# Optimization experiments

Hardware: AMD Instinct MI355X
Metric: run time of the kernel (lower is better)

## Reference

```python
import jax, jax.numpy as jnp
import numpy as np

B, DIM, HEADS, H, W = 4, 64, 8, 512, 512


def _conv(x, w, groups=1):
    # NCHW x, OIHW w, stride 1, SAME padding (padding=k//2 in torch)
    return jax.lax.conv_general_dilated(
        x, w, (1, 1), 'SAME', feature_group_count=groups,
        dimension_numbers=('NCHW', 'OIHW', 'NCHW'))


def _dwt_haar(x):
    # single-level orthonormal haar on even-sized NCHW input
    a = x[..., 0::2, 0::2]; b = x[..., 0::2, 1::2]
    c = x[..., 1::2, 0::2]; d = x[..., 1::2, 1::2]
    LL = (a + b + c + d) * 0.5
    LH = (-a - b + c + d) * 0.5
    HL = (-a + b - c + d) * 0.5
    HH = (a - b - c + d) * 0.5
    return LL, LH, HL, HH


def _idwt_haar(LL, LH, HL, HH):
    a = (LL - LH - HL + HH) * 0.5
    b = (LL - LH + HL - HH) * 0.5
    c = (LL + LH - HL - HH) * 0.5
    d = (LL + LH + HL + HH) * 0.5
    Bn, C, h, w = LL.shape
    even = jnp.stack([a, b], -1).reshape(Bn, C, h, 2 * w)  # rows 0::2
    odd = jnp.stack([c, d], -1).reshape(Bn, C, h, 2 * w)   # rows 1::2
    return jnp.stack([even, odd], -2).reshape(Bn, C, 2 * h, 2 * w)


def _l2norm(x, eps=1e-12):
    n = jnp.sqrt(jnp.sum(x * x, axis=-1, keepdims=True))
    return x / jnp.maximum(n, eps)


def setup_inputs() -> dict:
    key = jax.random.key(0)
    ks = jax.random.split(key, 8)
    def w(k, shape):
        fan_in = shape[1] * shape[2] * shape[3]
        return jax.random.normal(k, shape, jnp.float32) * (1.0 / np.sqrt(fan_in))
    return {
        'x': jax.random.normal(ks[0], (B, DIM, H, W), jnp.float32),
        'w_hc1': w(ks[1], (2 * DIM, DIM, 3, 3)),        # groups=2 over 2*dim channels
        'w_hc2': w(ks[2], (DIM, 2 * DIM, 1, 1)),
        'w_ho': w(ks[3], (3 * DIM, DIM, 3, 3)),          # groups=3 over 3*dim channels
        'w_qkv': w(ks[4], (3 * DIM, DIM, 1, 1)),
        'w_dw': w(ks[5], (3 * DIM, 1, 3, 3)),            # depthwise, groups=3*dim
        'w_proj': w(ks[6], (DIM, DIM, 1, 1)),
        'temperature': jnp.ones((HEADS, 1, 1), jnp.float32),
    }


def reference(x, w_hc1, w_hc2, w_ho, w_qkv, w_dw, w_proj, temperature):
    LL, LH, HL, HH = _dwt_haar(x)

    # high-frequency (LH,HL) filter branch
    hv = jnp.concatenate([LH, HL], axis=1)
    filter_hv = jax.nn.relu(_conv(jax.nn.relu(_conv(hv, w_hc1, groups=2)), w_hc2))

    # qkv from LL: 1x1 conv then depthwise 3x3
    qkv = _conv(_conv(LL, w_qkv), w_dw, groups=3 * DIM)
    q, k, v = jnp.split(qkv, 3, axis=1)
    b, c, h, w = q.shape
    v = v * filter_hv + v

    ch = c // HEADS
    q = q.reshape(b, HEADS, ch, h * w)
    k = k.reshape(b, HEADS, ch, h * w)
    v = v.reshape(b, HEADS, ch, h * w)
    q = _l2norm(q)
    k = _l2norm(k)

    attn = jnp.einsum('bhcn,bhdn->bhcd', q, k) * temperature  # [b,heads,ch,ch]
    attn = jax.nn.softmax(attn, axis=-1)
    out = jnp.einsum('bhcd,bhdn->bhcn', attn, v).reshape(b, c, h, w)
    out = _conv(out, w_proj)

    # high-frequency output branch
    yh = jax.nn.relu(_conv(jnp.concatenate([LH, HL, HH], axis=1), w_ho, groups=3))
    LH2, HL2, HH2 = jnp.split(yh, 3, axis=1)

    return _idwt_haar(out, LH2, HL2, HH2)
```

## Files before the change

### kernel.cpp

```cpp
#include <hip/hip_runtime.h>
#include <hip/hip_bf16.h>

#define BN 4
#define DIM 64
#define NHEADS 8
#define HH 256
#define WH 256
#define NP (HH*WH)
#define HF 512
#define WF 512

#define PD 258
#define PROW (PD*64)
#define PPLANE ((size_t)PD*PD*64)

typedef __attribute__((ext_vector_type(8))) short bfx8;
typedef __attribute__((ext_vector_type(8))) unsigned short u16x8;
typedef __attribute__((ext_vector_type(4))) float f32x4;

static __device__ __forceinline__ short f2bf(float f) {
    unsigned u = __float_as_uint(f);
    unsigned r = (u + 0x7FFFu + ((u >> 16) & 1u)) >> 16;
    return (short)r;
}
static __device__ __forceinline__ float bfu(unsigned short u) {
    return __uint_as_float((unsigned)u << 16);
}

__global__ __launch_bounds__(256) void k_ring(unsigned short* __restrict__ tiled) {
    int plane = blockIdx.x;
    char* base = (char*)(tiled + (size_t)plane * PPLANE);
    const int ROWB = PROW * 2;
    for (int k = threadIdx.x; k < 8224; k += 256) {
        char* dst;
        if (k < 2064) dst = base + (size_t)k * 16;
        else if (k < 4128) dst = base + (size_t)257 * ROWB + (size_t)(k - 2064) * 16;
        else if (k < 6176) { int r = (k - 4128) >> 3, s = (k - 4128) & 7;
            dst = base + (size_t)(r + 1) * ROWB + (size_t)s * 16; }
        else { int r = (k - 6176) >> 3, s = (k - 6176) & 7;
            dst = base + (size_t)(r + 1) * ROWB + 257 * 128 + (size_t)s * 16; }
        *(uint4*)dst = (uint4){0, 0, 0, 0};
    }
}

__global__ __launch_bounds__(256) void k_dwt(const float* __restrict__ x,
                                             unsigned short* __restrict__ LLT,
                                             unsigned short* __restrict__ tiled) {
    __shared__ unsigned short lds[3 * 128 * 64] __attribute__((aligned(16)));
    const int tid = threadIdx.x;
    const int pid = blockIdx.x;
    const int b = blockIdx.y;
    const int y0 = (pid >> 4) * 8, x0 = (pid & 15) * 16;
    const int quad = tid & 127;
    const int qy = quad >> 4, qx = quad & 15;
    const int gy = y0 + qy, gx = x0 + qx;
    const int ich = tid >> 7;
    const int tile_ll = (y0 >> 4) * 16 + (x0 >> 4);
    const int inner = ((gy & 15) << 4) + (gx & 15);
    unsigned short* llbase = LLT + ((size_t)(b * 256 + tile_ll) * 256 + inner) * 64;

#pragma unroll 4
    for (int it = 0; it < 16; ++it) {
        int ic = it * 4 + ich * 2;
        unsigned g = (((unsigned)(ic >> 3)) + (unsigned)gx + 2u * (unsigned)gy) & 7u;
        unsigned swz = (unsigned)quad * 64 + (g << 3) + (unsigned)(ic & 7);
        unsigned pk[3], pll;
#pragma unroll
        for (int s = 0; s < 2; ++s) {
            const float* px = x + (((size_t)(b * 64 + ic + s) * HF) + 2 * gy) * WF + 2 * gx;
            float2 e0 = *(const float2*)px;
            float2 e1 = *(const float2*)(px + WF);
            float a = e0.x, bb = e0.y, c = e1.x, d = e1.y;
            unsigned ll = (unsigned short)f2bf(( a + bb + c + d) * 0.5f);
            unsigned lh = (unsigned short)f2bf((-a - bb + c + d) * 0.5f);
            unsigned hl = (unsigned short)f2bf((-a + bb - c + d) * 0.5f);
            unsigned hh = (unsigned short)f2bf(( a - bb - c + d) * 0.5f);
            if (s == 0) { pll = ll; pk[0] = lh; pk[1] = hl; pk[2] = hh; }
            else { pll |= ll << 16; pk[0] |= lh << 16; pk[1] |= hl << 16; pk[2] |= hh << 16; }
        }
        *(unsigned*)&lds[swz]          = pk[0];
        *(unsigned*)&lds[8192 + swz]   = pk[1];
        *(unsigned*)&lds[16384 + swz]  = pk[2];
        unsigned gll = (((unsigned)(ic >> 3)) + (unsigned)inner) & 7u;
        *(unsigned*)&llbase[(gll << 3) + (unsigned)(ic & 7)] = pll;
    }
    __syncthreads();
#pragma unroll
    for (int it = 0; it < 12; ++it) {
        int cch = tid + it * 256;
        int p = cch >> 10, rem = cch & 1023;
        int row = rem >> 7, col = rem & 127;
        unsigned short* dst = tiled + ((size_t)(b * 3 + p) * PD + (y0 + row + 1)) * PROW
                                    + (size_t)(x0 + 1) * 64 + (size_t)col * 8;
        *(uint4*)dst = *(const uint4*)((const char*)lds + (size_t)cch * 16);
    }
}

__global__ __launch_bounds__(256) void k_repack(const float* __restrict__ w,
                                                short* __restrict__ wrep, int total) {
    int t = blockIdx.x * 256 + threadIdx.x;
    if (t >= total) return;
    unsigned g   = (unsigned)t / 36864u;
    unsigned r1  = (unsigned)t % 36864u;
    unsigned tap = r1 / 4096u;
    unsigned r2  = r1 % 4096u;
    unsigned icb = r2 / 512u;
    unsigned r3  = r2 % 512u;
    unsigned oc  = r3 >> 3;
    unsigned j   = r3 & 7u;
    unsigned ic  = icb * 8u + j;
    wrep[t] = f2bf(w[(((size_t)g * 64 + oc) * 64 + ic) * 9 + tap]);
}

template <int CIN, int OC>
__global__ __launch_bounds__(256) void k_repack1(const float* __restrict__ w,
                                                 short* __restrict__ wrep) {
    int t = blockIdx.x * 256 + threadIdx.x;
    if (t >= CIN * OC) return;
    constexpr int KB = CIN / 8;
    int j = t & 7;
    int gr = t >> 3;
    int o16 = gr & 15;
    int X = gr >> 4;
    int icb = X % KB;
    int oct = X / KB;
    int oc = oct * 16 + o16, ic = icb * 8 + j;
    wrep[t] = f2bf(w[(size_t)oc * CIN + ic]);
}

template <int LAYOUT>
__global__ __launch_bounds__(256) void k_gconv3x3_mfma(const unsigned short* __restrict__ tiled,
                                                       const bfx8* __restrict__ wr,
                                                       unsigned short* __restrict__ out, int OC) {
    __shared__ short lds_in[324 * 64] __attribute__((aligned(16)));
    const int tid = threadIdx.x;
    const int l = tid & 63, wv = tid >> 6;
    const int tile = blockIdx.x;
    const int x0 = (tile & 15) * 16, y0 = (tile >> 4) * 16;
    const int g = blockIdx.y, b = blockIdx.z;
    const unsigned short* src = tiled + (size_t)(b * 3 + g) * PPLANE;

#pragma unroll
    for (int it = 0; it < 10; ++it) {
        int cch = it * 256 + tid;
        unsigned row = (unsigned)cch / 144u, col = (unsigned)cch % 144u;
        const unsigned short* ga = src + (size_t)(y0 + row) * PROW + (size_t)x0 * 64 + (size_t)col * 8;
        __builtin_amdgcn_global_load_lds(
            (const __attribute__((address_space(1))) void*)ga,
            (__attribute__((address_space(3))) void*)((char*)lds_in + (size_t)(it * 256 + wv * 64) * 16),
            16, 0, 0);
    }
    if (tid < 32) {
        int cch = 2560 + tid;
        unsigned row = (unsigned)cch / 144u, col = (unsigned)cch % 144u;
        const unsigned short* ga = src + (size_t)(y0 + row) * PROW + (size_t)x0 * 64 + (size_t)col * 8;
        *(uint4*)((char*)lds_in + (size_t)cch * 16) = *(const uint4*)ga;
    }
    __syncthreads();

    f32x4 acc[4][4];
#pragma unroll
    for (int i = 0; i < 4; ++i)
#pragma unroll
        for (int j = 0; j < 4; ++j) acc[i][j] = (f32x4){0.f, 0.f, 0.f, 0.f};

    const int lx = l & 15, lq = l >> 4;
#pragma unroll
    for (int c = 0; c < 2; ++c) {
        const int icb = c * 4 + lq;
#pragma unroll
        for (int tap = 0; tap < 9; ++tap) {
            const int dy = tap / 3, dx = tap % 3;
            const size_t wbase = ((size_t)(g * 9 + tap) * 8 + icb) * 64 + lx;
            bfx8 b0 = wr[wbase];
            bfx8 b1 = wr[wbase + 16];
            bfx8 b2 = wr[wbase + 32];
            bfx8 b3 = wr[wbase + 48];
#pragma unroll
            for (int pg = 0; pg < 4; ++pg) {
                int hy = wv * 4 + pg + dy, hx = lx + dx;
                int hp = hy * 18 + hx;
                const bfx8* ap = (const bfx8*)&lds_in[hp * 64 + (((icb + hx + 2 * hy + 5) & 7) << 3)];
                bfx8 a = *ap;
                acc[pg][0] = __builtin_amdgcn_mfma_f32_16x16x32_bf16(a, b0, acc[pg][0], 0, 0, 0);
                acc[pg][1] = __builtin_amdgcn_mfma_f32_16x16x32_bf16(a, b1, acc[pg][1], 0, 0, 0);
                acc[pg][2] = __builtin_amdgcn_mfma_f32_16x16x32_bf16(a, b2, acc[pg][2], 0, 0, 0);
                acc[pg][3] = __builtin_amdgcn_mfma_f32_16x16x32_bf16(a, b3, acc[pg][3], 0, 0, 0);
            }
        }
    }

#pragma unroll
    for (int pg = 0; pg < 4; ++pg) {
#pragma unroll
        for (int ocg = 0; ocg < 4; ++ocg) {
            f32x4 v = acc[pg][ocg];
            if (LAYOUT == 0) {
                unsigned short* op = out + ((size_t)b * OC + g * 64 + ocg * 16 + lx) * NP
                                         + (size_t)(y0 + wv * 4 + pg) * WH + x0 + lq * 4;
                ushort4 s4;
                s4.x = (unsigned short)f2bf(fmaxf(v.x, 0.f));
                s4.y = (unsigned short)f2bf(fmaxf(v.y, 0.f));
                s4.z = (unsigned short)f2bf(fmaxf(v.z, 0.f));
                s4.w = (unsigned short)f2bf(fmaxf(v.w, 0.f));
                *(ushort4*)op = s4;
            } else {
                int icT = g * 64 + ocg * 16 + lx;
                int g16 = icT >> 3;
                unsigned short* tb = out + ((size_t)(b * 256 + tile) * 256) * 128;
                int innerb = (wv * 4 + pg) * 16 + lq * 4;
                float vr[4] = {v.x, v.y, v.z, v.w};
#pragma unroll
                for (int r = 0; r < 4; ++r) {
                    int inn = innerb + r;
                    tb[(size_t)inn * 128 + (((g16 + inn) & 15) << 3) + (icT & 7)] =
                        (unsigned short)f2bf(fmaxf(vr[r], 0.f));
                }
            }
        }
    }
}

template <int CIN, int OC, bool RELU>
__global__ __launch_bounds__(256) void k_conv1x1_mfma(const unsigned short* __restrict__ inT,
                                                      const bfx8* __restrict__ wr,
                                                      unsigned short* __restrict__ out) {
    constexpr int KB = CIN / 8;
    constexpr int KC = CIN / 32;
    constexpr int NOCT = OC / 16;
    __shared__ short ldsA[256 * CIN] __attribute__((aligned(16)));
    const int tid = threadIdx.x;
    const int l = tid & 63, wv = tid >> 6;
    const int tile = blockIdx.x, b = blockIdx.y;
    const unsigned short* src = inT + ((size_t)(b * 256 + tile) * 256) * CIN;
    constexpr int ITER = (256 * CIN / 8) / 256;
#pragma unroll
    for (int it = 0; it < ITER; ++it) {
        int cc = it * 256 + tid;
        __builtin_amdgcn_global_load_lds(
            (const __attribute__((address_space(1))) void*)(src + (size_t)cc * 8),
            (__attribute__((address_space(3))) void*)((char*)ldsA + (size_t)(it * 256 + wv * 64) * 16),
            16, 0, 0);
    }
    __syncthreads();

    const int lx = l & 15, lq = l >> 4;
    const int x0 = (tile & 15) * 16, y0 = (tile >> 4) * 16;
#pragma unroll
    for (int o4 = 0; o4 < NOCT / 4; ++o4) {
        f32x4 acc[4][4];
#pragma unroll
        for (int i = 0; i < 4; ++i)
#pragma unroll
            for (int j = 0; j < 4; ++j) acc[i][j] = (f32x4){0.f, 0.f, 0.f, 0.f};
#pragma unroll
        for (int c = 0; c < KC; ++c) {
            const int icb = c * 4 + lq;
            bfx8 bf[4];
#pragma unroll
            for (int ot = 0; ot < 4; ++ot)
                bf[ot] = wr[(size_t)(((o4 * 4 + ot) * KB + icb) * 16) + lx];
#pragma unroll
            for (int pg = 0; pg < 4; ++pg) {
                int inner = (wv * 4 + pg) * 16 + lx;
                const bfx8* ap = (const bfx8*)&ldsA[inner * CIN + (((icb + inner) & (KB - 1)) << 3)];
                bfx8 a = *ap;
                acc[pg][0] = __builtin_amdgcn_mfma_f32_16x16x32_bf16(a, bf[0], acc[pg][0], 0, 0, 0);
                acc[pg][1] = __builtin_amdgcn_mfma_f32_16x16x32_bf16(a, bf[1], acc[pg][1], 0, 0, 0);
                acc[pg][2] = __builtin_amdgcn_mfma_f32_16x16x32_bf16(a, bf[2], acc[pg][2], 0, 0, 0);
                acc[pg][3] = __builtin_amdgcn_mfma_f32_16x16x32_bf16(a, bf[3], acc[pg][3], 0, 0, 0);
            }
        }
#pragma unroll
        for (int pg = 0; pg < 4; ++pg)
#pragma unroll
            for (int ot = 0; ot < 4; ++ot) {
                int oc = (o4 * 4 + ot) * 16 + lx;
                unsigned short* op = out + ((size_t)b * OC + oc) * NP
                                         + (size_t)(y0 + wv * 4 + pg) * WH + x0 + lq * 4;
                f32x4 v = acc[pg][ot];
                ushort4 s4;
                s4.x = (unsigned short)f2bf(RELU ? fmaxf(v.x, 0.f) : v.x);
                s4.y = (unsigned short)f2bf(RELU ? fmaxf(v.y, 0.f) : v.y);
                s4.z = (unsigned short)f2bf(RELU ? fmaxf(v.z, 0.f) : v.z);
                s4.w = (unsigned short)f2bf(RELU ? fmaxf(v.w, 0.f) : v.w);
                *(ushort4*)op = s4;
            }
    }
}

__global__ __launch_bounds__(256) void k_dwconv(const unsigned short* __restrict__ in,
                                                const float* __restrict__ w,
                                                const unsigned short* __restrict__ filt,
                                                unsigned short* __restrict__ out) {
    int p8 = blockIdx.x * 256 + threadIdx.x;
    int bc = blockIdx.y;
    int c = bc % 192, b = bc / 192;
    int y = p8 >> 5, x0 = (p8 & 31) * 8;
    const unsigned short* ip = in + (size_t)bc * NP;
    float wv[9];
#pragma unroll
    for (int t = 0; t < 9; ++t) wv[t] = w[c * 9 + t];

    float f[3][10];
#pragma unroll
    for (int r = 0; r < 3; ++r) {
        int yy = y + r - 1;
        if (yy < 0 || yy >= HH) {
#pragma unroll
            for (int k = 0; k < 10; ++k) f[r][k] = 0.f;
        } else {
            const unsigned short* rp = ip + (size_t)yy * WH;
            u16x8 C = *(const u16x8*)(rp + x0);
#pragma unroll
            for (int k = 0; k < 8; ++k) f[r][k + 1] = bfu(C[k]);
            f[r][0] = (x0 > 0) ? bfu(rp[x0 - 1]) : 0.f;
            f[r][9] = (x0 < 248) ? bfu(rp[x0 + 8]) : 0.f;
        }
    }
    float o[8];
#pragma unroll
    for (int k = 0; k < 8; ++k) {
        float s = 0.f;
#pragma unroll
        for (int r = 0; r < 3; ++r)
#pragma unroll
            for (int dx = 0; dx < 3; ++dx)
                s = fmaf(f[r][k + dx], wv[r * 3 + dx], s);
        o[k] = s;
    }
    if (c >= 128) {
        const unsigned short* fp = filt + ((size_t)b * 64 + (c - 128)) * NP + (size_t)y * WH + x0;
        u16x8 f8 = *(const u16x8*)fp;
#pragma unroll
        for (int k = 0; k < 8; ++k) o[k] = fmaf(o[k], bfu(f8[k]), o[k]);
    }
    u16x8 s8;
#pragma unroll
    for (int k = 0; k < 8; ++k) s8[k] = (unsigned short)f2bf(o[k]);
    *(u16x8*)(out + (size_t)bc * NP + (size_t)y * WH + x0) = s8;
}

__global__ __launch_bounds__(256) void k_attn_dot(const unsigned short* __restrict__ qkv,
                                                  float* __restrict__ praw,
                                                  float* __restrict__ praw2) {
    int bhd = blockIdx.x, sp = blockIdx.y;
    int b = bhd >> 3, hd = bhd & 7;
    const unsigned short* qb = qkv + ((size_t)b * 192 + hd * 8) * NP;
    const unsigned short* kb = qkv + ((size_t)b * 192 + 64 + hd * 8) * NP;
    float acc[64], acc2[16];
#pragma unroll
    for (int i = 0; i < 64; ++i) acc[i] = 0.f;
#pragma unroll
    for (int i = 0; i < 16; ++i) acc2[i] = 0.f;
    int n0 = sp * (NP / 8);
    for (int n = n0 + threadIdx.x; n < n0 + NP / 8; n += 256) {
        float qv[8], kv[8];
#pragma unroll
        for (int c2 = 0; c2 < 8; ++c2) qv[c2] = bfu(qb[(size_t)c2 * NP + n]);
#pragma unroll
        for (int d2 = 0; d2 < 8; ++d2) kv[d2] = bfu(kb[(size_t)d2 * NP + n]);
#pragma unroll
        for (int c2 = 0; c2 < 8; ++c2) {
            acc2[c2] = fmaf(qv[c2], qv[c2], acc2[c2]);
#pragma unroll
            for (int d2 = 0; d2 < 8; ++d2)
                acc[c2 * 8 + d2] = fmaf(qv[c2], kv[d2], acc[c2 * 8 + d2]);
        }
#pragma unroll
        for (int d2 = 0; d2 < 8; ++d2) acc2[8 + d2] = fmaf(kv[d2], kv[d2], acc2[8 + d2]);
    }
    __shared__ float red[4][64];
#pragma unroll
    for (int i = 0; i < 64; ++i) {
        float v = acc[i];
#pragma unroll
        for (int off = 32; off; off >>= 1) v += __shfl_down(v, off);
        if ((threadIdx.x & 63) == 0) red[threadIdx.x >> 6][i] = v;
    }
    __syncthreads();
    if (threadIdx.x < 64)
        praw[((size_t)sp * 32 + bhd) * 64 + threadIdx.x] =
            red[0][threadIdx.x] + red[1][threadIdx.x] + red[2][threadIdx.x] + red[3][threadIdx.x];
    __syncthreads();
#pragma unroll
    for (int i = 0; i < 16; ++i) {
        float v = acc2[i];
#pragma unroll
        for (int off = 32; off; off >>= 1) v += __shfl_down(v, off);
        if ((threadIdx.x & 63) == 0) red[threadIdx.x >> 6][i] = v;
    }
    __syncthreads();
    if (threadIdx.x < 16)
        praw2[((size_t)sp * 32 + bhd) * 16 + threadIdx.x] =
            red[0][threadIdx.x] + red[1][threadIdx.x] + red[2][threadIdx.x] + red[3][threadIdx.x];
}

__global__ __launch_bounds__(64) void k_attn_soft(const float* __restrict__ praw,
                                                  const float* __restrict__ praw2,
                                                  const float* __restrict__ temp,
                                                  float* __restrict__ attn) {
    int bhd = blockIdx.x;
    int hd = bhd & 7;
    int t = threadIdx.x, c = t >> 3, d = t & 7;
    float s = 0.f, sq = 0.f, sk = 0.f;
    for (int sp = 0; sp < 8; ++sp) {
        s  += praw[((size_t)sp * 32 + bhd) * 64 + t];
        sq += praw2[((size_t)sp * 32 + bhd) * 16 + c];
        sk += praw2[((size_t)sp * 32 + bhd) * 16 + 8 + d];
    }
    float nq = fmaxf(sqrtf(sq), 1e-12f);
    float nk = fmaxf(sqrtf(sk), 1e-12f);
    s = s / (nq * nk) * temp[hd];
    __shared__ float sm[64];
    __shared__ float se[64];
    sm[t] = s;
    __syncthreads();
    float mx = -1e30f;
#pragma unroll
    for (int dd = 0; dd < 8; ++dd) mx = fmaxf(mx, sm[c * 8 + dd]);
    float e = __expf(s - mx);
    se[t] = e;
    __syncthreads();
    float sum = 0.f;
#pragma unroll
    for (int dd = 0; dd < 8; ++dd) sum += se[c * 8 + dd];
    attn[(size_t)bhd * 64 + t] = e / sum;
}

__global__ __launch_bounds__(256) void k_attnout_idwt(const unsigned short* __restrict__ qkv,
                                                      const float* __restrict__ attn,
                                                      const float* __restrict__ wproj,
                                                      const unsigned short* __restrict__ yh,
                                                      float* __restrict__ out) {
    __shared__ float wsh[64 * 64];
    __shared__ float ash[512];
    const int tid = threadIdx.x;
    const int b = blockIdx.y;
    const int p = blockIdx.x * 256 + tid;
#pragma unroll
    for (int it = 0; it < 16; ++it) wsh[tid + it * 256] = wproj[tid + it * 256];
#pragma unroll
    for (int it = 0; it < 2; ++it) ash[tid + it * 256] = attn[(size_t)b * 512 + tid + it * 256];
    __syncthreads();

    float av[64];
    const unsigned short* vb = qkv + ((size_t)b * 192 + 128) * NP + p;
#pragma unroll
    for (int hd = 0; hd < 8; ++hd) {
        float vv[8];
#pragma unroll
        for (int d = 0; d < 8; ++d) vv[d] = bfu(vb[(size_t)(hd * 8 + d) * NP]);
#pragma unroll
        for (int c2 = 0; c2 < 8; ++c2) {
            float s = 0.f;
#pragma unroll
            for (int d = 0; d < 8; ++d) s = fmaf(ash[hd * 64 + c2 * 8 + d], vv[d], s);
            av[hd * 8 + c2] = s;
        }
    }
    const int i = p >> 8, j = p & 255;
    const unsigned short* yb = yh + (size_t)b * 192 * NP + p;
    float* ob = out + ((size_t)b * 64 * HF + 2 * i) * WF + 2 * j;
    for (int c = 0; c < 64; ++c) {
        float s = 0.f;
#pragma unroll
        for (int ic = 0; ic < 64; ++ic) s = fmaf(av[ic], wsh[c * 64 + ic], s);
        float LHv = bfu(yb[(size_t)c * NP]);
        float HLv = bfu(yb[(size_t)(c + 64) * NP]);
        float HHv = bfu(yb[(size_t)(c + 128) * NP]);
        float* oc_ = ob + (size_t)c * HF * WF;
        *(float2*)oc_        = make_float2((s - LHv - HLv + HHv) * 0.5f, (s - LHv + HLv - HHv) * 0.5f);
        *(float2*)(oc_ + WF) = make_float2((s + LHv - HLv - HHv) * 0.5f, (s + LHv + HLv + HHv) * 0.5f);
    }
}

extern "C" void kernel_launch(void* const* d_in, const int* in_sizes, int n_in,
                              void* d_out, int out_size, void* d_ws, size_t ws_size,
                              hipStream_t stream) {
    const float* x      = (const float*)d_in[0];
    const float* w_hc1  = (const float*)d_in[1];
    const float* w_hc2  = (const float*)d_in[2];
    const float* w_ho   = (const float*)d_in[3];
    const float* w_qkv  = (const float*)d_in[4];
    const float* w_dw   = (const float*)d_in[5];
    const float* w_proj = (const float*)d_in[6];
    const float* temp   = (const float*)d_in[7];
    float* out = (float*)d_out;

    char* base = (char*)d_ws;
    unsigned short* TILED = (unsigned short*)(base + 0);
    unsigned short* LLT   = (unsigned short*)(base + 102242304ULL);
    unsigned short* YH    = (unsigned short*)(base + 135796736ULL);
    unsigned short* T1T   = (unsigned short*)(base + 236460032ULL);
    unsigned short* FILT  = (unsigned short*)(base + 303568896ULL);
    unsigned short* QKV0  = (unsigned short*)(base + 337123328ULL);
    unsigned short* QKV   = (unsigned short*)(base + 437786624ULL);
    float*          PRAW  = (float*)(base + 538449920ULL);
    float*          PRAW2 = (float*)(base + 538515456ULL);
    float*          ATTN  = (float*)(base + 538531840ULL);
    short* WREP_HO  = (short*)(base + 538540032ULL);
    short* WREP_HC1 = (short*)(base + 538761216ULL);
    short* WREP_HC2 = (short*)(base + 538908672ULL);
    short* WREP_QKV = (short*)(base + 538925056ULL);

    k_ring<<<12, 256, 0, stream>>>(TILED);
    k_repack<<<(3 * 36864 + 255) / 256, 256, 0, stream>>>(w_ho, WREP_HO, 3 * 36864);
    k_repack<<<(2 * 36864 + 255) / 256, 256, 0, stream>>>(w_hc1, WREP_HC1, 2 * 36864);
    k_repack1<128, 64><<<32, 256, 0, stream>>>(w_hc2, WREP_HC2);
    k_repack1<64, 192><<<48, 256, 0, stream>>>(w_qkv, WREP_QKV);
    k_dwt<<<dim3(512, BN), 256, 0, stream>>>(x, LLT, TILED);
    k_gconv3x3_mfma<0><<<dim3(256, 3, BN), 256, 0, stream>>>(TILED, (const bfx8*)WREP_HO, YH, 192);
    k_gconv3x3_mfma<1><<<dim3(256, 2, BN), 256, 0, stream>>>(TILED, (const bfx8*)WREP_HC1, T1T, 128);
    k_conv1x1_mfma<128, 64, true><<<dim3(256, BN), 256, 0, stream>>>(T1T, (const bfx8*)WREP_HC2, FILT);
    k_conv1x1_mfma<64, 192, false><<<dim3(256, BN), 256, 0, stream>>>(LLT, (const bfx8*)WREP_QKV, QKV0);
    k_dwconv<<<dim3(32, BN * 192), 256, 0, stream>>>(QKV0, w_dw, FILT, QKV);
    k_attn_dot<<<dim3(32, 8), 256, 0, stream>>>(QKV, PRAW, PRAW2);
    k_attn_soft<<<32, 64, 0, stream>>>(PRAW, PRAW2, temp, ATTN);
    k_attnout_idwt<<<dim3(256, BN), 256, 0, stream>>>(QKV, ATTN, w_proj, YH, out);
}
```

Baseline: 642.5 us.

## Fuse qkv 1x1 conv with depthwise 3x3 and merge setup kernels

The LL band is now written into a zero-padded, swizzled plane layout so one kernel can load an 18x18 halo tile, run the 1x1 qkv conv with MFMA into LDS, and apply the depthwise 3x3 plus the filter modulation before writing QKV. This removes the QKV0 intermediate round trip through global memory and one kernel launch. The ring-zeroing and weight repacks are merged into a single setup kernel to cut launch overhead. In exchange, the 1x1 conv is recomputed on halo pixels, the depthwise loop is per-channel scalar work out of LDS, and high LDS use may lower occupancy.

```diff
diff --git a/kernel.cpp b/kernel.cpp
--- a/kernel.cpp
+++ b/kernel.cpp
@@ -27,25 +27,64 @@
     return __uint_as_float((unsigned)u << 16);
 }
 
-__global__ __launch_bounds__(256) void k_ring(unsigned short* __restrict__ tiled) {
-    int plane = blockIdx.x;
-    char* base = (char*)(tiled + (size_t)plane * PPLANE);
-    const int ROWB = PROW * 2;
-    for (int k = threadIdx.x; k < 8224; k += 256) {
-        char* dst;
-        if (k < 2064) dst = base + (size_t)k * 16;
-        else if (k < 4128) dst = base + (size_t)257 * ROWB + (size_t)(k - 2064) * 16;
-        else if (k < 6176) { int r = (k - 4128) >> 3, s = (k - 4128) & 7;
-            dst = base + (size_t)(r + 1) * ROWB + (size_t)s * 16; }
-        else { int r = (k - 6176) >> 3, s = (k - 6176) & 7;
-            dst = base + (size_t)(r + 1) * ROWB + 257 * 128 + (size_t)s * 16; }
-        *(uint4*)dst = (uint4){0, 0, 0, 0};
+__global__ __launch_bounds__(256) void k_setup(unsigned short* __restrict__ tiled16,
+                                               const float* __restrict__ w_ho,
+                                               const float* __restrict__ w_hc1,
+                                               const float* __restrict__ w_hc2,
+                                               const float* __restrict__ w_qkv,
+                                               short* __restrict__ wrHO,
+                                               short* __restrict__ wrHC1,
+                                               short* __restrict__ wrHC2,
+                                               short* __restrict__ wrQKV) {
+    int bx = blockIdx.x, tid = threadIdx.x;
+    if (bx < 16) {
+        char* base = (char*)(tiled16 + (size_t)bx * PPLANE);
+        const int ROWB = PROW * 2;
+        for (int k = tid; k < 8224; k += 256) {
+            char* dst;
+            if (k < 2064) dst = base + (size_t)k * 16;
+            else if (k < 4128) dst = base + (size_t)257 * ROWB + (size_t)(k - 2064) * 16;
+            else if (k < 6176) { int r = (k - 4128) >> 3, s = (k - 4128) & 7;
+                dst = base + (size_t)(r + 1) * ROWB + (size_t)s * 16; }
+            else { int r = (k - 6176) >> 3, s = (k - 6176) & 7;
+                dst = base + (size_t)(r + 1) * ROWB + 257 * 128 + (size_t)s * 16; }
+            *(uint4*)dst = (uint4){0, 0, 0, 0};
+        }
+        return;
+    }
+    if (bx < 16 + 432 + 288) {
+        const float* w = (bx < 448) ? w_ho : w_hc1;
+        short* wrep = (bx < 448) ? wrHO : wrHC1;
+        int t = (bx - ((bx < 448) ? 16 : 448)) * 256 + tid;
+        unsigned g   = (unsigned)t / 36864u;
+        unsigned r1  = (unsigned)t % 36864u;
+        unsigned tap = r1 / 4096u;
+        unsigned r2  = r1 % 4096u;
+        unsigned icb = r2 / 512u;
+        unsigned r3  = r2 % 512u;
+        unsigned oc  = r3 >> 3;
+        unsigned j   = r3 & 7u;
+        wrep[t] = f2bf(w[(((size_t)g * 64 + oc) * 64 + icb * 8u + j) * 9 + tap]);
+        return;
+    }
+    if (bx < 16 + 432 + 288 + 32) {
+        int t = (bx - 736) * 256 + tid;
+        int j = t & 7, gr = t >> 3, o16 = gr & 15, X = gr >> 4;
+        int icb = X % 16, oct = X / 16;
+        wrHC2[t] = f2bf(w_hc2[(size_t)(oct * 16 + o16) * 128 + icb * 8 + j]);
+        return;
+    }
+    {
+        int t = (bx - 768) * 256 + tid;
+        int j = t & 7, gr = t >> 3, o16 = gr & 15, X = gr >> 4;
+        int icb = X % 8, oct = X / 8;
+        wrQKV[t] = f2bf(w_qkv[(size_t)(oct * 16 + o16) * 64 + icb * 8 + j]);
     }
 }
 
 __global__ __launch_bounds__(256) void k_dwt(const float* __restrict__ x,
-                                             unsigned short* __restrict__ LLT,
-                                             unsigned short* __restrict__ tiled) {
+                                             unsigned short* __restrict__ tiled,
+                                             unsigned short* __restrict__ llp) {
     __shared__ unsigned short lds[3 * 128 * 64] __attribute__((aligned(16)));
     const int tid = threadIdx.x;
     const int pid = blockIdx.x;
@@ -55,9 +94,7 @@
     const int qy = quad >> 4, qx = quad & 15;
     const int gy = y0 + qy, gx = x0 + qx;
     const int ich = tid >> 7;
-    const int tile_ll = (y0 >> 4) * 16 + (x0 >> 4);
-    const int inner = ((gy & 15) << 4) + (gx & 15);
-    unsigned short* llbase = LLT + ((size_t)(b * 256 + tile_ll) * 256 + inner) * 64;
+    unsigned short* llb = llp + (size_t)b * PPLANE + ((size_t)(gy + 1) * PD + (gx + 1)) * 64;
 
 #pragma unroll 4
     for (int it = 0; it < 16; ++it) {
@@ -81,8 +118,7 @@
         *(unsigned*)&lds[swz]          = pk[0];
         *(unsigned*)&lds[8192 + swz]   = pk[1];
         *(unsigned*)&lds[16384 + swz]  = pk[2];
-        unsigned gll = (((unsigned)(ic >> 3)) + (unsigned)inner) & 7u;
-        *(unsigned*)&llbase[(gll << 3) + (unsigned)(ic & 7)] = pll;
+        *(unsigned*)&llb[(g << 3) + (unsigned)(ic & 7)] = pll;
     }
     __syncthreads();
 #pragma unroll
@@ -94,38 +130,6 @@
                                     + (size_t)(x0 + 1) * 64 + (size_t)col * 8;
         *(uint4*)dst = *(const uint4*)((const char*)lds + (size_t)cch * 16);
     }
-}
-
-__global__ __launch_bounds__(256) void k_repack(const float* __restrict__ w,
-                                                short* __restrict__ wrep, int total) {
-    int t = blockIdx.x * 256 + threadIdx.x;
-    if (t >= total) return;
-    unsigned g   = (unsigned)t / 36864u;
-    unsigned r1  = (unsigned)t % 36864u;
-    unsigned tap = r1 / 4096u;
-    unsigned r2  = r1 % 4096u;
-    unsigned icb = r2 / 512u;
-    unsigned r3  = r2 % 512u;
-    unsigned oc  = r3 >> 3;
-    unsigned j   = r3 & 7u;
-    unsigned ic  = icb * 8u + j;
-    wrep[t] = f2bf(w[(((size_t)g * 64 + oc) * 64 + ic) * 9 + tap]);
-}
-
-template <int CIN, int OC>
-__global__ __launch_bounds__(256) void k_repack1(const float* __restrict__ w,
-                                                 short* __restrict__ wrep) {
-    int t = blockIdx.x * 256 + threadIdx.x;
-    if (t >= CIN * OC) return;
-    constexpr int KB = CIN / 8;
-    int j = t & 7;
-    int gr = t >> 3;
-    int o16 = gr & 15;
-    int X = gr >> 4;
-    int icb = X % KB;
-    int oct = X / KB;
-    int oc = oct * 16 + o16, ic = icb * 8 + j;
-    wrep[t] = f2bf(w[(size_t)oc * CIN + ic]);
 }
 
 template <int LAYOUT>
@@ -289,56 +293,140 @@
     }
 }
 
-__global__ __launch_bounds__(256) void k_dwconv(const unsigned short* __restrict__ in,
-                                                const float* __restrict__ w,
-                                                const unsigned short* __restrict__ filt,
-                                                unsigned short* __restrict__ out) {
-    int p8 = blockIdx.x * 256 + threadIdx.x;
-    int bc = blockIdx.y;
-    int c = bc % 192, b = bc / 192;
-    int y = p8 >> 5, x0 = (p8 & 31) * 8;
-    const unsigned short* ip = in + (size_t)bc * NP;
-    float wv[9];
-#pragma unroll
-    for (int t = 0; t < 9; ++t) wv[t] = w[c * 9 + t];
-
-    float f[3][10];
-#pragma unroll
-    for (int r = 0; r < 3; ++r) {
-        int yy = y + r - 1;
-        if (yy < 0 || yy >= HH) {
-#pragma unroll
-            for (int k = 0; k < 10; ++k) f[r][k] = 0.f;
-        } else {
-            const unsigned short* rp = ip + (size_t)yy * WH;
-            u16x8 C = *(const u16x8*)(rp + x0);
-#pragma unroll
-            for (int k = 0; k < 8; ++k) f[r][k + 1] = bfu(C[k]);
-            f[r][0] = (x0 > 0) ? bfu(rp[x0 - 1]) : 0.f;
-            f[r][9] = (x0 < 248) ? bfu(rp[x0 + 8]) : 0.f;
-        }
-    }
-    float o[8];
-#pragma unroll
-    for (int k = 0; k < 8; ++k) {
-        float s = 0.f;
-#pragma unroll
-        for (int r = 0; r < 3; ++r)
-#pragma unroll
-            for (int dx = 0; dx < 3; ++dx)
-                s = fmaf(f[r][k + dx], wv[r * 3 + dx], s);
-        o[k] = s;
-    }
-    if (c >= 128) {
-        const unsigned short* fp = filt + ((size_t)b * 64 + (c - 128)) * NP + (size_t)y * WH + x0;
-        u16x8 f8 = *(const u16x8*)fp;
-#pragma unroll
-        for (int k = 0; k < 8; ++k) o[k] = fmaf(o[k], bfu(f8[k]), o[k]);
-    }
-    u16x8 s8;
-#pragma unroll
-    for (int k = 0; k < 8; ++k) s8[k] = (unsigned short)f2bf(o[k]);
-    *(u16x8*)(out + (size_t)bc * NP + (size_t)y * WH + x0) = s8;
+__global__ __launch_bounds__(256) void k_qkv_fused(const unsigned short* __restrict__ llp,
+                                                   const bfx8* __restrict__ wrq,
+                                                   const float* __restrict__ wdw,
+                                                   const unsigned short* __restrict__ filt,
+                                                   unsigned short* __restrict__ qkv) {
+    __shared__ short ldsA[336 * 64] __attribute__((aligned(16)));
+    __shared__ float ldsW[192 * 9];
+    const int tid = threadIdx.x;
+    const int l = tid & 63, wv = tid >> 6;
+    const int tile = blockIdx.x, b = blockIdx.y;
+    const int x0 = (tile & 15) * 16, y0 = (tile >> 4) * 16;
+    const unsigned short* src = llp + (size_t)b * PPLANE;
+
+#pragma unroll
+    for (int it = 0; it < 10; ++it) {
+        int cch = it * 256 + tid;
+        unsigned row = (unsigned)cch / 144u, col = (unsigned)cch % 144u;
+        const unsigned short* ga = src + (size_t)(y0 + row) * PROW + (size_t)x0 * 64 + (size_t)col * 8;
+        __builtin_amdgcn_global_load_lds(
+            (const __attribute__((address_space(1))) void*)ga,
+            (__attribute__((address_space(3))) void*)((char*)ldsA + (size_t)(it * 256 + wv * 64) * 16),
+            16, 0, 0);
+    }
+    if (tid < 32) {
+        int cch = 2560 + tid;
+        unsigned row = (unsigned)cch / 144u, col = (unsigned)cch % 144u;
+        const unsigned short* ga = src + (size_t)(y0 + row) * PROW + (size_t)x0 * 64 + (size_t)col * 8;
+        *(uint4*)((char*)ldsA + (size_t)cch * 16) = *(const uint4*)ga;
+    }
+    for (int k = tid; k < 1728; k += 256) ldsW[k] = wdw[k];
+    __syncthreads();
+
+    const int lx = l & 15, lq = l >> 4;
+    bfx8 af[6][2];
+#pragma unroll
+    for (int m = 0; m < 6; ++m) {
+        int mt = wv + 4 * m;
+        if (mt < 21) {
+            int hp = mt * 16 + lx;
+            int hy = hp / 18, hx = hp - hy * 18;
+#pragma unroll
+            for (int kc = 0; kc < 2; ++kc) {
+                int icb = kc * 4 + lq;
+                af[m][kc] = *(const bfx8*)&ldsA[hp * 64 + (((icb + hx + 2 * hy + 5) & 7) << 3)];
+            }
+        }
+    }
+    __syncthreads();
+
+    for (int g3 = 0; g3 < 3; ++g3) {
+        bfx8 bw[2][4];
+#pragma unroll
+        for (int kc = 0; kc < 2; ++kc)
+#pragma unroll
+            for (int nt = 0; nt < 4; ++nt)
+                bw[kc][nt] = wrq[(size_t)(((g3 * 4 + nt) * 8) + kc * 4 + lq) * 16 + lx];
+#pragma unroll
+        for (int m = 0; m < 6; ++m) {
+            int mt = wv + 4 * m;
+            if (mt < 21) {
+                f32x4 acc[4];
+#pragma unroll
+                for (int nt = 0; nt < 4; ++nt) acc[nt] = (f32x4){0.f, 0.f, 0.f, 0.f};
+#pragma unroll
+                for (int kc = 0; kc < 2; ++kc) {
+                    bfx8 a = af[m][kc];
+#pragma unroll
+                    for (int nt = 0; nt < 4; ++nt)
+                        acc[nt] = __builtin_amdgcn_mfma_f32_16x16x32_bf16(a, bw[kc][nt], acc[nt], 0, 0, 0);
+                }
+#pragma unroll
+                for (int nt = 0; nt < 4; ++nt) {
+                    int ocl = nt * 16 + lx;
+                    float vr[4] = {acc[nt].x, acc[nt].y, acc[nt].z, acc[nt].w};
+#pragma unroll
+                    for (int r = 0; r < 4; ++r) {
+                        int hp2 = mt * 16 + lq * 4 + r;
+                        int hy2 = hp2 / 18, hx2 = hp2 - hy2 * 18;
+                        ldsA[hp2 * 64 + ((((ocl >> 3) + hx2 + 2 * hy2) & 7) << 3) + (ocl & 7)] =
+                            f2bf(vr[r]);
+                    }
+                }
+            }
+        }
+        __syncthreads();
+        {
+            const int ch = l, chg = g3 * 64 + ch;
+            float w9[9];
+#pragma unroll
+            for (int t = 0; t < 9; ++t) w9[t] = ldsW[chg * 9 + t];
+#pragma unroll
+            for (int yy = 0; yy < 4; ++yy) {
+                int y = wv * 4 + yy;
+                float ln[3][18];
+#pragma unroll
+                for (int hr = 0; hr < 3; ++hr) {
+                    int hy = y + hr;
+#pragma unroll
+                    for (int hx = 0; hx < 18; ++hx)
+                        ln[hr][hx] = bfu((unsigned short)ldsA[(hy * 18 + hx) * 64 +
+                                         ((((ch >> 3) + hx + 2 * hy) & 7) << 3) + (ch & 7)]);
+                }
+                float ox[16];
+#pragma unroll
+                for (int xx = 0; xx < 16; ++xx) {
+                    float s = 0.f;
+#pragma unroll
+                    for (int hr = 0; hr < 3; ++hr)
+#pragma unroll
+                        for (int dx = 0; dx < 3; ++dx)
+                            s = fmaf(ln[hr][xx + dx], w9[hr * 3 + dx], s);
+                    ox[xx] = s;
+                }
+                if (g3 == 2) {
+                    const unsigned short* fp = filt + ((size_t)b * 64 + ch) * NP
+                                                    + (size_t)(y0 + y) * WH + x0;
+                    u16x8 f0 = *(const u16x8*)fp;
+                    u16x8 f1 = *(const u16x8*)(fp + 8);
+#pragma unroll
+                    for (int k = 0; k < 8; ++k) ox[k]     = fmaf(ox[k],     bfu(f0[k]), ox[k]);
+#pragma unroll
+                    for (int k = 0; k < 8; ++k) ox[8 + k] = fmaf(ox[8 + k], bfu(f1[k]), ox[8 + k]);
+                }
+                u16x8 s0, s1;
+#pragma unroll
+                for (int k = 0; k < 8; ++k) { s0[k] = (unsigned short)f2bf(ox[k]);
+                                              s1[k] = (unsigned short)f2bf(ox[8 + k]); }
+                unsigned short* op = qkv + ((size_t)b * 192 + chg) * NP + (size_t)(y0 + y) * WH + x0;
+                *(u16x8*)op = s0;
+                *(u16x8*)(op + 8) = s1;
+            }
+        }
+        __syncthreads();
+    }
 }
 
 __global__ __launch_bounds__(256) void k_attn_dot(const unsigned short* __restrict__ qkv,
@@ -490,31 +578,26 @@
 
     char* base = (char*)d_ws;
     unsigned short* TILED = (unsigned short*)(base + 0);
-    unsigned short* LLT   = (unsigned short*)(base + 102242304ULL);
-    unsigned short* YH    = (unsigned short*)(base + 135796736ULL);
-    unsigned short* T1T   = (unsigned short*)(base + 236460032ULL);
-    unsigned short* FILT  = (unsigned short*)(base + 303568896ULL);
-    unsigned short* QKV0  = (unsigned short*)(base + 337123328ULL);
-    unsigned short* QKV   = (unsigned short*)(base + 437786624ULL);
-    float*          PRAW  = (float*)(base + 538449920ULL);
-    float*          PRAW2 = (float*)(base + 538515456ULL);
-    float*          ATTN  = (float*)(base + 538531840ULL);
-    short* WREP_HO  = (short*)(base + 538540032ULL);
-    short* WREP_HC1 = (short*)(base + 538761216ULL);
-    short* WREP_HC2 = (short*)(base + 538908672ULL);
-    short* WREP_QKV = (short*)(base + 538925056ULL);
-
-    k_ring<<<12, 256, 0, stream>>>(TILED);
-    k_repack<<<(3 * 36864 + 255) / 256, 256, 0, stream>>>(w_ho, WREP_HO, 3 * 36864);
-    k_repack<<<(2 * 36864 + 255) / 256, 256, 0, stream>>>(w_hc1, WREP_HC1, 2 * 36864);
-    k_repack1<128, 64><<<32, 256, 0, stream>>>(w_hc2, WREP_HC2);
-    k_repack1<64, 192><<<48, 256, 0, stream>>>(w_qkv, WREP_QKV);
-    k_dwt<<<dim3(512, BN), 256, 0, stream>>>(x, LLT, TILED);
+    unsigned short* LLP   = (unsigned short*)(base + 102242304ULL);
+    unsigned short* YH    = (unsigned short*)(base + 136323072ULL);
+    unsigned short* T1T   = (unsigned short*)(base + 236986368ULL);
+    unsigned short* FILT  = (unsigned short*)(base + 304095232ULL);
+    unsigned short* QKV   = (unsigned short*)(base + 337649664ULL);
+    float*          PRAW  = (float*)(base + 438312960ULL);
+    float*          PRAW2 = (float*)(base + 438378496ULL);
+    float*          ATTN  = (float*)(base + 438394880ULL);
+    short* WREP_HO  = (short*)(base + 438403072ULL);
+    short* WREP_HC1 = (short*)(base + 438624256ULL);
+    short* WREP_HC2 = (short*)(base + 438771712ULL);
+    short* WREP_QKV = (short*)(base + 438788096ULL);
+
+    k_setup<<<816, 256, 0, stream>>>(TILED, w_ho, w_hc1, w_hc2, w_qkv,
+                                     WREP_HO, WREP_HC1, WREP_HC2, WREP_QKV);
+    k_dwt<<<dim3(512, BN), 256, 0, stream>>>(x, TILED, LLP);
     k_gconv3x3_mfma<0><<<dim3(256, 3, BN), 256, 0, stream>>>(TILED, (const bfx8*)WREP_HO, YH, 192);
     k_gconv3x3_mfma<1><<<dim3(256, 2, BN), 256, 0, stream>>>(TILED, (const bfx8*)WREP_HC1, T1T, 128);
     k_conv1x1_mfma<128, 64, true><<<dim3(256, BN), 256, 0, stream>>>(T1T, (const bfx8*)WREP_HC2, FILT);
-    k_conv1x1_mfma<64, 192, false><<<dim3(256, BN), 256, 0, stream>>>(LLT, (const bfx8*)WREP_QKV, QKV0);
-    k_dwconv<<<dim3(32, BN * 192), 256, 0, stream>>>(QKV0, w_dw, FILT, QKV);
+    k_qkv_fused<<<dim3(256, BN), 256, 0, stream>>>(LLP, (const bfx8*)WREP_QKV, w_dw, FILT, QKV);
     k_attn_dot<<<dim3(32, 8), 256, 0, stream>>>(QKV, PRAW, PRAW2);
     k_attn_soft<<<32, 64, 0, stream>>>(PRAW, PRAW2, temp, ATTN);
     k_attnout_idwt<<<dim3(256, BN), 256, 0, stream>>>(QKV, ATTN, w_proj, YH, out);
```

New measurement: 613.5 us. 1.05x faster.
